# Performance work log

Hardware: AMD Instinct MI355X
Metric: run time of the kernel (lower is better)

## Reference

```python
import jax, jax.numpy as jnp
import numpy as np

N_NODES = 100000
N_EDGES = 1600000
N_FEAT = 128
HIDDEN = 128
N_GRAPHS = 64
N_CLASSES = 10
BN_EPS = 1e-5


def setup_inputs() -> dict:
    key = jax.random.key(0)
    ks = jax.random.split(key, 24)
    glorot = lambda k, o, i: jax.random.normal(k, (o, i), jnp.float32) * (1.0 / np.sqrt(i))
    inp = {
        'x': jax.random.normal(ks[0], (N_NODES, N_FEAT), jnp.float32),
        'edge_index': jax.random.randint(ks[1], (2, N_EDGES), 0, N_NODES, jnp.int64),
        'batch': jnp.sort(jax.random.randint(ks[2], (N_NODES,), 0, N_GRAPHS, jnp.int64)),
        # GCNConv(128 -> 128)
        'gcn_w': glorot(ks[3], HIDDEN, N_FEAT),
        'gcn_b': jnp.zeros((HIDDEN,), jnp.float32),
        # SAGEConv layers 1, 2: lin_l (aggregated, with bias) + lin_r (root, no bias)
        'sage1_wl': glorot(ks[4], HIDDEN, HIDDEN),
        'sage1_bl': jnp.zeros((HIDDEN,), jnp.float32),
        'sage1_wr': glorot(ks[5], HIDDEN, HIDDEN),
        'sage2_wl': glorot(ks[6], HIDDEN, HIDDEN),
        'sage2_bl': jnp.zeros((HIDDEN,), jnp.float32),
        'sage2_wr': glorot(ks[7], HIDDEN, HIDDEN),
        # ClassifierBase: 128 -> 200 -> 100 -> 50 -> 10
        'clf_w0': glorot(ks[8], 200, HIDDEN), 'clf_b0': jnp.zeros((200,), jnp.float32),
        'clf_w1': glorot(ks[9], 100, 200), 'clf_b1': jnp.zeros((100,), jnp.float32),
        'clf_w2': glorot(ks[10], 50, 100), 'clf_b2': jnp.zeros((50,), jnp.float32),
        'clf_w3': glorot(ks[11], N_CLASSES, 50), 'clf_b3': jnp.zeros((N_CLASSES,), jnp.float32),
        # BatchNorm1d (eval mode, running_mean=0, running_var=1)
        'bn0_g': jnp.ones((200,), jnp.float32), 'bn0_b': jnp.zeros((200,), jnp.float32),
        'bn1_g': jnp.ones((100,), jnp.float32), 'bn1_b': jnp.zeros((100,), jnp.float32),
        'bn2_g': jnp.ones((50,), jnp.float32), 'bn2_b': jnp.zeros((50,), jnp.float32),
    }
    return inp


def _gcn_conv(x, src, dst, W, b):
    # PyG GCNConv: add self loops, symmetric deg^{-1/2} normalization
    xw = x @ W.T                                                  # [N, H]
    ones = jnp.ones(src.shape[0], xw.dtype)
    deg = jax.ops.segment_sum(ones, dst, num_segments=N_NODES) + 1.0  # self loops
    dinv = jax.lax.rsqrt(deg)
    norm = dinv[src] * dinv[dst]                                  # [E]
    out = jax.ops.segment_sum(xw[src] * norm[:, None], dst, num_segments=N_NODES)
    out = out + xw * (dinv * dinv)[:, None]                       # self-loop term deg^{-1}
    return out + b


def _sage_conv(x, src, dst, Wl, bl, Wr):
    # PyG SAGEConv (mean aggr): lin_l(mean_{j->i} x_j) + lin_r(x_i)
    ones = jnp.ones(src.shape[0], x.dtype)
    cnt = jax.ops.segment_sum(ones, dst, num_segments=N_NODES)
    agg = jax.ops.segment_sum(x[src], dst, num_segments=N_NODES)
    agg = agg / jnp.maximum(cnt, 1.0)[:, None]
    return agg @ Wl.T + bl + x @ Wr.T


def _bn_eval(h, g, b):
    # eval-mode BatchNorm1d with running_mean=0, running_var=1
    return h * (g / np.sqrt(1.0 + BN_EPS)) + b


def reference(x, edge_index, batch, gcn_w, gcn_b,
              sage1_wl, sage1_bl, sage1_wr, sage2_wl, sage2_bl, sage2_wr,
              clf_w0, clf_b0, clf_w1, clf_b1, clf_w2, clf_b2, clf_w3, clf_b3,
              bn0_g, bn0_b, bn1_g, bn1_b, bn2_g, bn2_b):
    src, dst = edge_index[0], edge_index[1]
    h = _gcn_conv(x, src, dst, gcn_w, gcn_b)          # act_func is None -> no activation
    h = _sage_conv(h, src, dst, sage1_wl, sage1_bl, sage1_wr)
    h = _sage_conv(h, src, dst, sage2_wl, sage2_bl, sage2_wr)
    # global mean pool over graphs
    gcnt = jax.ops.segment_sum(jnp.ones(h.shape[0], h.dtype), batch, num_segments=N_GRAPHS)
    g = jax.ops.segment_sum(h, batch, num_segments=N_GRAPHS) / jnp.maximum(gcnt, 1.0)[:, None]
    # ClassifierBase (eval: dropout inactive), tanh activation
    g = jnp.tanh(_bn_eval(g @ clf_w0.T + clf_b0, bn0_g, bn0_b))
    g = jnp.tanh(_bn_eval(g @ clf_w1.T + clf_b1, bn1_g, bn1_b))
    g = jnp.tanh(_bn_eval(g @ clf_w2.T + clf_b2, bn2_g, bn2_b))
    logits = g @ clf_w3.T + clf_b3
    return jax.nn.softmax(logits, axis=1)             # [B, n_classes]
```

## Files before the change

kernel.cpp:

```cpp
#include <hip/hip_runtime.h>

#define N_NODES 100000
#define N_EDGES 1600000
#define NGRAPH 64
#define NBIN 391
#define EPB 2560
#define NBLK 625
#define WBLK 200
#define CAPB 6144
#define CAPP 7168
#define PSPLIT 8

typedef short s8v __attribute__((ext_vector_type(8)));
typedef float f4v __attribute__((ext_vector_type(4)));
typedef float f2v __attribute__((ext_vector_type(2)));

__device__ __forceinline__ float bflo(unsigned u) { return __uint_as_float(u << 16); }
__device__ __forceinline__ float bfhi(unsigned u) { return __uint_as_float(u & 0xffff0000u); }
__device__ __forceinline__ unsigned short f2bf(float f) {
    unsigned u = __float_as_uint(f);
    u += 0x7fffu + ((u >> 16) & 1u);
    return (unsigned short)(u >> 16);
}
__device__ __forceinline__ float bf2f(unsigned short h) { return __uint_as_float(((unsigned)h) << 16); }
__device__ __forceinline__ unsigned pk(float lo, float hi) {
    return (unsigned)f2bf(lo) | ((unsigned)f2bf(hi) << 16);
}
__device__ __forceinline__ float ldv(const void* p, int i, int f32) {
    return f32 ? ((const float*)p)[i] : bf2f(((const unsigned short*)p)[i]);
}
__device__ __forceinline__ f2v up2(unsigned u) {
    f2v t; t.x = bflo(u); t.y = bfhi(u); return t;
}

__global__ __launch_bounds__(256) void k_prep(const unsigned short* __restrict__ x,
                                              const int* __restrict__ ei,
                                              const int* __restrict__ batch,
                                              int* __restrict__ flags,
                                              int* __restrict__ binCur,
                                              int* __restrict__ gstart,
                                              float* __restrict__ pbuf,
                                              float* __restrict__ wbuf,
                                              unsigned* __restrict__ xcvt,
                                              unsigned* __restrict__ staging,
                                              const void* w0, const void* w1,
                                              const void* w2, const void* w3,
                                              const void* b0, const void* bn0g, const void* bn0b,
                                              const void* b1, const void* bn1g, const void* bn1b,
                                              const void* b2, const void* bn2g, const void* bn2b,
                                              const void* b3) {
    int tid = threadIdx.x, bid = blockIdx.x;
    if (bid < NBLK) {
        __shared__ int cnt[NBIN];
        __shared__ int lofs[NBIN];
        __shared__ int curL[NBIN];
        __shared__ int basg[NBIN];
        __shared__ int sA[512], sB[512];
        __shared__ int sbuf[EPB];
        __shared__ int dbuf[EPB];
        __shared__ unsigned ebuf[EPB];
        __shared__ unsigned short bbuf[EPB];
        __shared__ int p64;
        if (tid == 0) p64 = 0;
        for (int i = tid; i < NBIN; i += 256) cnt[i] = 0;
        __syncthreads();
        if (ei[2 * (tid * 5000) + 1] == 0) atomicAdd(&p64, 1);
        __syncthreads();
        int i64 = (p64 == 256);
        int base = bid * EPB;
        #pragma unroll
        for (int k = 0; k < EPB / 512; ++k) {
            int e = base + k * 512 + tid * 2;
            int s0, s1, d0, d1;
            if (i64) {
                uint4 vs = *(const uint4*)(ei + 2 * (size_t)e);
                uint4 vd = *(const uint4*)(ei + 2 * (size_t)(N_EDGES + e));
                s0 = (int)vs.x; s1 = (int)vs.z;
                d0 = (int)vd.x; d1 = (int)vd.z;
            } else {
                int2 vs = *(const int2*)(ei + (size_t)e);
                int2 vd = *(const int2*)(ei + (size_t)N_EDGES + e);
                s0 = vs.x; s1 = vs.y;
                d0 = vd.x; d1 = vd.y;
            }
            int l = k * 512 + tid * 2;
            sbuf[l] = s0; sbuf[l + 1] = s1;
            dbuf[l] = d0; dbuf[l + 1] = d1;
            if ((unsigned)d0 < N_NODES) atomicAdd(&cnt[d0 >> 8], 1);
            if ((unsigned)d1 < N_NODES) atomicAdd(&cnt[d1 >> 8], 1);
        }
        __syncthreads();
        for (int k = tid; k < 512; k += 256) sA[k] = (k < NBIN) ? cnt[k] : 0;
        __syncthreads();
        int* src = sA;
        int* dst = sB;
        for (int off = 1; off < 512; off <<= 1) {
            for (int k = tid; k < 512; k += 256)
                dst[k] = src[k] + ((k >= off) ? src[k - off] : 0);
            __syncthreads();
            int* t = src; src = dst; dst = t;
        }
        int totE = src[NBIN - 1];
        for (int i = tid; i < NBIN; i += 256) {
            int excl = src[i] - cnt[i];
            lofs[i] = excl;
            curL[i] = excl;
            basg[i] = i * CAPB + (cnt[i] ? atomicAdd(&binCur[i], cnt[i]) : 0);
        }
        __syncthreads();
        #pragma unroll
        for (int k = 0; k < EPB / 256; ++k) {
            int l = k * 256 + tid;
            int d = dbuf[l];
            int s = sbuf[l];
            if ((unsigned)d < N_NODES) {
                s = min(max(s, 0), N_NODES - 1);
                int p = atomicAdd(&curL[d >> 8], 1);
                ebuf[p] = ((unsigned)(d & 255) << 20) | (unsigned)s;
                bbuf[p] = (unsigned short)(d >> 8);
            }
        }
        __syncthreads();
        for (int i = tid; i < totE; i += 256) {
            int bb = bbuf[i];
            int p = basg[bb] + (i - lofs[bb]);
            if (p < (bb + 1) * CAPB) staging[p] = ebuf[i];
        }
        return;
    }
    int wb = bid - NBLK;
    __shared__ int c0, c2;
    if (tid == 0) { c0 = 0; c2 = 0; }
    __syncthreads();
    unsigned short hh = x[tid * 37];
    int e = (hh >> 7) & 0xFF;
    if (e >= 100 && e <= 150) atomicAdd(&c0, 1);
    if (wb == 0 && batch[2 * (tid * 193) + 1] == 0) atomicAdd(&c2, 1);
    __syncthreads();
    int f = (c0 == 256) ? 0 : 1;
    int i = wb * 256 + tid;
    if (i < 25600) wbuf[i] = ldv(w0, i, f);
    else if (i < 45600) wbuf[i] = ldv(w1, i - 25600, f);
    else if (i < 50600) wbuf[i] = ldv(w2, i - 45600, f);
    else if (i < 51100) wbuf[i] = ldv(w3, i - 50600, f);
    if (f) {
        for (int id = wb * 256 + tid; id < N_NODES * 64; id += WBLK * 256) {
            float2 u = ((const float2*)x)[id];
            xcvt[id] = pk(u.x, u.y);
        }
    }
    if (wb != 0) return;
    int b64 = (c2 == 256) ? 1 : 0;
    if (tid == 0) {
        flags[0] = f;
        flags[1] = 0;
        flags[2] = b64;
    }
    if (tid <= NGRAPH) {
        int g = tid, lo = 0, hi = N_NODES;
        while (lo < hi) {
            int mid = (lo + hi) >> 1;
            int v = b64 ? batch[2 * mid] : batch[mid];
            if (v < g) lo = mid + 1;
            else hi = mid;
        }
        gstart[g] = lo;
    }
    const float invs = rsqrtf(1.0f + 1e-5f);
    if (tid < 200) {
        float a = ldv(bn0g, tid, f) * invs;
        pbuf[tid] = a;
        pbuf[200 + tid] = ldv(b0, tid, f) * a + ldv(bn0b, tid, f);
    }
    if (tid < 100) {
        float a = ldv(bn1g, tid, f) * invs;
        pbuf[400 + tid] = a;
        pbuf[500 + tid] = ldv(b1, tid, f) * a + ldv(bn1b, tid, f);
    }
    if (tid < 50) {
        float a = ldv(bn2g, tid, f) * invs;
        pbuf[600 + tid] = a;
        pbuf[650 + tid] = ldv(b2, tid, f) * a + ldv(bn2b, tid, f);
    }
    if (tid < 10) pbuf[700 + tid] = ldv(b3, tid, f);
}

__global__ __launch_bounds__(256) void k_csr(const unsigned* __restrict__ staging,
                                             const int* __restrict__ binCur,
                                             int2* __restrict__ rse,
                                             float* __restrict__ dinv,
                                             int* __restrict__ colidx,
                                             unsigned* __restrict__ padA,
                                             unsigned* __restrict__ padB) {
    __shared__ int deg[256];
    __shared__ int s[256];
    __shared__ int cur[256];
    __shared__ int colbuf[CAPP];
    int b = blockIdx.x, tid = threadIdx.x;
    int n0 = b << 8;
    int nend = min(256, N_NODES - n0);
    int runStart = b * CAPB;
    int outStart = b * CAPP;
    int runLen = min(binCur[b], CAPB);
    deg[tid] = 0;
    for (int i = tid; i < CAPP; i += 256) colbuf[i] = N_NODES;
    __syncthreads();
    for (int i = tid; i < runLen; i += 256)
        atomicAdd(&deg[staging[runStart + i] >> 20], 1);
    __syncthreads();
    int myDeg = deg[tid];
    int pdeg = (myDeg + 15) & ~15;
    s[tid] = pdeg;
    __syncthreads();
    for (int off = 1; off < 256; off <<= 1) {
        int x2 = (tid >= off) ? s[tid - off] : 0;
        __syncthreads();
        s[tid] += x2;
        __syncthreads();
    }
    int incl = s[tid];
    int lrs = incl - pdeg;
    if (tid < nend) {
        rse[n0 + tid] = make_int2(outStart + lrs, outStart + lrs + myDeg);
        dinv[n0 + tid] = rsqrtf((float)myDeg + 1.0f);
    }
    cur[tid] = lrs;
    __syncthreads();
    for (int i = tid; i < runLen; i += 256) {
        unsigned e = staging[runStart + i];
        int p = atomicAdd(&cur[e >> 20], 1);
        if (p < CAPP) colbuf[p] = (int)(e & 0xFFFFF);
    }
    __syncthreads();
    int ptot = min(s[255], CAPP);
    for (int i = tid; i < ptot; i += 256) colidx[outStart + i] = colbuf[i];
    if (b == 0) {
        if (tid < 64) {
            padA[(size_t)N_NODES * 64 + tid] = 0u;
            padB[(size_t)N_NODES * 64 + tid] = 0u;
        }
        if (tid == 0) dinv[N_NODES] = 0.f;
    }
}

template <int MODE>
__global__ __launch_bounds__(256) void k_agg(const uint4* __restrict__ xsA,
                                             const uint4* __restrict__ xsB,
                                             const int2* __restrict__ rse,
                                             const float* __restrict__ dinv,
                                             unsigned* __restrict__ out,
                                             const int* __restrict__ col,
                                             const int* __restrict__ flags) {
    int lane = threadIdx.x & 63;
    int wid = blockIdx.x * 4 + (threadIdx.x >> 6);
    int glane = lane & 15, grp = lane >> 4;
    const uint4* xs = (MODE == 0) ? (flags[0] ? xsB : xsA) : xsA;
    #pragma unroll
    for (int h = 0; h < 2; ++h) {
        int nodeA = wid * 4 + h * 2;
        int nodeB = nodeA + 1;
        int2 ra = rse[nodeA];
        int2 rb = rse[nodeB];
        int degA = ra.y - ra.x, degB = rb.y - rb.x;
        int pendA = ra.x + ((degA + 15) & ~15);
        int pendB = rb.x + ((degB + 15) & ~15);
        int rounds = max(pendA - ra.x, pendB - rb.x) >> 4;
        int baseA = ra.x + grp * 4, baseB = rb.x + grp * 4;
        f2v aA0 = {0.f, 0.f}, aA1 = {0.f, 0.f}, aA2 = {0.f, 0.f}, aA3 = {0.f, 0.f};
        f2v aB0 = {0.f, 0.f}, aB1 = {0.f, 0.f}, aB2 = {0.f, 0.f}, aB3 = {0.f, 0.f};
        uint4 selfA = make_uint4(0u, 0u, 0u, 0u), selfB = make_uint4(0u, 0u, 0u, 0u);
        float diA = 0.f, diB = 0.f;
        if (MODE == 0) {
            selfA = xs[(size_t)nodeA * 16u + glane]; diA = dinv[nodeA];
            selfB = xs[(size_t)nodeB * 16u + glane]; diB = dinv[nodeB];
        }
        for (int r = 0; r < rounds; ++r) {
            int4 ca = *(const int4*)(col + baseA);
            int4 cb = *(const int4*)(col + baseB);
            if (baseA >= pendA) { ca.x = N_NODES; ca.y = N_NODES; ca.z = N_NODES; ca.w = N_NODES; }
            if (baseB >= pendB) { cb.x = N_NODES; cb.y = N_NODES; cb.z = N_NODES; cb.w = N_NODES; }
            baseA += 16; baseB += 16;
            float d0, d1, d2, d3, e0, e1, e2, e3;
            if (MODE == 0) {
                d0 = dinv[ca.x]; d1 = dinv[ca.y]; d2 = dinv[ca.z]; d3 = dinv[ca.w];
                e0 = dinv[cb.x]; e1 = dinv[cb.y]; e2 = dinv[cb.z]; e3 = dinv[cb.w];
                ca.x = min(ca.x, N_NODES - 1); ca.y = min(ca.y, N_NODES - 1);
                ca.z = min(ca.z, N_NODES - 1); ca.w = min(ca.w, N_NODES - 1);
                cb.x = min(cb.x, N_NODES - 1); cb.y = min(cb.y, N_NODES - 1);
                cb.z = min(cb.z, N_NODES - 1); cb.w = min(cb.w, N_NODES - 1);
            }
            uint4 u0 = xs[(size_t)(unsigned)ca.x * 16u + glane];
            uint4 u1 = xs[(size_t)(unsigned)ca.y * 16u + glane];
            uint4 u2 = xs[(size_t)(unsigned)ca.z * 16u + glane];
            uint4 u3 = xs[(size_t)(unsigned)ca.w * 16u + glane];
            uint4 v0 = xs[(size_t)(unsigned)cb.x * 16u + glane];
            uint4 v1 = xs[(size_t)(unsigned)cb.y * 16u + glane];
            uint4 v2 = xs[(size_t)(unsigned)cb.z * 16u + glane];
            uint4 v3 = xs[(size_t)(unsigned)cb.w * 16u + glane];
            if (MODE == 0) {
                aA0 += d0 * up2(u0.x); aA1 += d0 * up2(u0.y); aA2 += d0 * up2(u0.z); aA3 += d0 * up2(u0.w);
                aA0 += d1 * up2(u1.x); aA1 += d1 * up2(u1.y); aA2 += d1 * up2(u1.z); aA3 += d1 * up2(u1.w);
                aA0 += d2 * up2(u2.x); aA1 += d2 * up2(u2.y); aA2 += d2 * up2(u2.z); aA3 += d2 * up2(u2.w);
                aA0 += d3 * up2(u3.x); aA1 += d3 * up2(u3.y); aA2 += d3 * up2(u3.z); aA3 += d3 * up2(u3.w);
                aB0 += e0 * up2(v0.x); aB1 += e0 * up2(v0.y); aB2 += e0 * up2(v0.z); aB3 += e0 * up2(v0.w);
                aB0 += e1 * up2(v1.x); aB1 += e1 * up2(v1.y); aB2 += e1 * up2(v1.z); aB3 += e1 * up2(v1.w);
                aB0 += e2 * up2(v2.x); aB1 += e2 * up2(v2.y); aB2 += e2 * up2(v2.z); aB3 += e2 * up2(v2.w);
                aB0 += e3 * up2(v3.x); aB1 += e3 * up2(v3.y); aB2 += e3 * up2(v3.z); aB3 += e3 * up2(v3.w);
            } else {
                aA0 += up2(u0.x); aA1 += up2(u0.y); aA2 += up2(u0.z); aA3 += up2(u0.w);
                aA0 += up2(u1.x); aA1 += up2(u1.y); aA2 += up2(u1.z); aA3 += up2(u1.w);
                aA0 += up2(u2.x); aA1 += up2(u2.y); aA2 += up2(u2.z); aA3 += up2(u2.w);
                aA0 += up2(u3.x); aA1 += up2(u3.y); aA2 += up2(u3.z); aA3 += up2(u3.w);
                aB0 += up2(v0.x); aB1 += up2(v0.y); aB2 += up2(v0.z); aB3 += up2(v0.w);
                aB0 += up2(v1.x); aB1 += up2(v1.y); aB2 += up2(v1.z); aB3 += up2(v1.w);
                aB0 += up2(v2.x); aB1 += up2(v2.y); aB2 += up2(v2.z); aB3 += up2(v2.w);
                aB0 += up2(v3.x); aB1 += up2(v3.y); aB2 += up2(v3.z); aB3 += up2(v3.w);
            }
        }
        float rA[8] = {aA0.x, aA0.y, aA1.x, aA1.y, aA2.x, aA2.y, aA3.x, aA3.y};
        float rB[8] = {aB0.x, aB0.y, aB1.x, aB1.y, aB2.x, aB2.y, aB3.x, aB3.y};
        #pragma unroll
        for (int i = 0; i < 8; ++i) {
            float v = rA[i];
            v += __shfl_xor(v, 16, 64);
            v += __shfl_xor(v, 32, 64);
            rA[i] = v;
            float w = rB[i];
            w += __shfl_xor(w, 16, 64);
            w += __shfl_xor(w, 32, 64);
            rB[i] = w;
        }
        if (MODE == 0) {
            float dA2 = diA * diA, dB2 = diB * diB;
            rA[0] = diA * rA[0] + dA2 * bflo(selfA.x); rA[1] = diA * rA[1] + dA2 * bfhi(selfA.x);
            rA[2] = diA * rA[2] + dA2 * bflo(selfA.y); rA[3] = diA * rA[3] + dA2 * bfhi(selfA.y);
            rA[4] = diA * rA[4] + dA2 * bflo(selfA.z); rA[5] = diA * rA[5] + dA2 * bfhi(selfA.z);
            rA[6] = diA * rA[6] + dA2 * bflo(selfA.w); rA[7] = diA * rA[7] + dA2 * bfhi(selfA.w);
            rB[0] = diB * rB[0] + dB2 * bflo(selfB.x); rB[1] = diB * rB[1] + dB2 * bfhi(selfB.x);
            rB[2] = diB * rB[2] + dB2 * bflo(selfB.y); rB[3] = diB * rB[3] + dB2 * bfhi(selfB.y);
            rB[4] = diB * rB[4] + dB2 * bflo(selfB.z); rB[5] = diB * rB[5] + dB2 * bfhi(selfB.z);
            rB[6] = diB * rB[6] + dB2 * bflo(selfB.w); rB[7] = diB * rB[7] + dB2 * bfhi(selfB.w);
        } else {
            float sA = 1.0f / fmaxf((float)degA, 1.0f);
            float sB = 1.0f / fmaxf((float)degB, 1.0f);
            #pragma unroll
            for (int i = 0; i < 8; ++i) { rA[i] *= sA; rB[i] *= sB; }
        }
        if (grp == 0) {
            uint4 o;
            o.x = pk(rA[0], rA[1]); o.y = pk(rA[2], rA[3]);
            o.z = pk(rA[4], rA[5]); o.w = pk(rA[6], rA[7]);
            *(uint4*)(out + (size_t)nodeA * 64 + glane * 4) = o;
            o.x = pk(rB[0], rB[1]); o.y = pk(rB[2], rB[3]);
            o.z = pk(rB[4], rB[5]); o.w = pk(rB[6], rB[7]);
            *(uint4*)(out + (size_t)nodeB * 64 + glane * 4) = o;
        }
    }
}

template <int DUAL>
__global__ __launch_bounds__(512) void k_gemm(const unsigned short* __restrict__ A0,
                                              const void* __restrict__ W0,
                                              const unsigned short* __restrict__ A1,
                                              const void* __restrict__ W1,
                                              const void* __restrict__ bias,
                                              unsigned short* __restrict__ out,
                                              const int* __restrict__ flags) {
    __shared__ __align__(16) unsigned short Ws[128][136];
    int f32 = flags[0];
    int tid = threadIdx.x;
    int lane = tid & 63;
    int wave = tid >> 6;
    int rowbase = blockIdx.x * 128;
    int lr = lane & 15, q = lane >> 4;
    int m0 = wave * 16;
    int arow = rowbase + m0 + lr;
    if (arow > N_NODES) arow = N_NODES;

    f4v acc[8];
    #pragma unroll
    for (int t = 0; t < 8; ++t) acc[t] = (f4v){0.f, 0.f, 0.f, 0.f};

    #pragma unroll
    for (int p = 0; p < (DUAL ? 2 : 1); ++p) {
        const unsigned short* Ap = p ? A1 : A0;
        const void* Wp = p ? W1 : W0;
        if (p) __syncthreads();
        if (!f32) {
            const unsigned short* Wf = (const unsigned short*)Wp;
            #pragma unroll
            for (int it = 0; it < 4; ++it) {
                int chunk = tid + it * 512;
                int r = chunk >> 4, c8 = (chunk & 15) * 8;
                *(uint4*)&Ws[r][c8] = *(const uint4*)(Wf + r * 128 + c8);
            }
        } else {
            const float* Wf = (const float*)Wp;
            #pragma unroll
            for (int it = 0; it < 8; ++it) {
                int chunk = tid + it * 512;
                int r = chunk >> 5, c4 = (chunk & 31) * 4;
                float4 v = *(const float4*)(Wf + r * 128 + c4);
                *(uint2*)&Ws[r][c4] = make_uint2(pk(v.x, v.y), pk(v.z, v.w));
            }
        }
        const unsigned short* Arp = Ap + (size_t)arow * 128;
        s8v a[4];
        #pragma unroll
        for (int k = 0; k < 4; ++k) a[k] = *(const s8v*)(Arp + k * 32 + q * 8);
        __syncthreads();
        #pragma unroll
        for (int k = 0; k < 4; ++k) {
            #pragma unroll
            for (int t = 0; t < 8; ++t) {
                s8v b = *(const s8v*)&Ws[t * 16 + lr][k * 32 + q * 8];
                acc[t] = __builtin_amdgcn_mfma_f32_16x16x32_bf16(a[k], b, acc[t], 0, 0, 0);
            }
        }
    }
    #pragma unroll
    for (int t = 0; t < 8; ++t) {
        int o = t * 16 + lr;
        float bv = ldv(bias, o, f32);
        #pragma unroll
        for (int j = 0; j < 4; ++j) {
            int m = rowbase + m0 + q * 4 + j;
            if (m < N_NODES) out[(size_t)m * 128 + o] = f2bf(acc[t][j] + bv);
        }
    }
}

__global__ __launch_bounds__(256) void k_pool2(const unsigned* __restrict__ h,
                                               const int* __restrict__ gstart,
                                               float* __restrict__ ppool) {
    __shared__ float part[4][128];
    int g = blockIdx.x / PSPLIT, sl = blockIdx.x % PSPLIT;
    int wave = threadIdx.x >> 6, lane = threadIdx.x & 63;
    int s0 = gstart[g], s1 = gstart[g + 1];
    int n = s1 - s0;
    int chunk = (n + PSPLIT - 1) / PSPLIT;
    int r0 = s0 + sl * chunk;
    int r1 = min(r0 + chunk, s1);
    float a0 = 0.f, a1 = 0.f;
    for (int r = r0 + wave; r < r1; r += 4) {
        unsigned u = h[(size_t)r * 64 + lane];
        a0 += bflo(u);
        a1 += bfhi(u);
    }
    part[wave][2 * lane] = a0;
    part[wave][2 * lane + 1] = a1;
    __syncthreads();
    int t = threadIdx.x;
    if (t < 128) {
        float s = part[0][t] + part[1][t] + part[2][t] + part[3][t];
        ppool[(size_t)blockIdx.x * 128 + t] = s;
    }
}

__global__ __launch_bounds__(256) void k_clf(const float* __restrict__ ppool,
                                             const int* __restrict__ gstart,
                                             const float* __restrict__ wbuf,
                                             const float* __restrict__ pbuf,
                                             void* outv, const int* __restrict__ flags) {
    __shared__ float gin[128];
    __shared__ float ha[200];
    __shared__ float hb[100];
    int b = blockIdx.x, t = threadIdx.x;
    if (t < 128) {
        float s = 0.f;
        #pragma unroll
        for (int k = 0; k < PSPLIT; ++k) s += ppool[(size_t)(b * PSPLIT + k) * 128 + t];
        int cnt = gstart[b + 1] - gstart[b];
        gin[t] = s / fmaxf((float)cnt, 1.0f);
    }
    __syncthreads();
    if (t < 200) {
        const float4* wr = (const float4*)(wbuf + t * 128);
        float s = 0.f;
        #pragma unroll
        for (int k = 0; k < 32; ++k) {
            float4 v = wr[k];
            s += v.x * gin[4 * k] + v.y * gin[4 * k + 1] + v.z * gin[4 * k + 2] + v.w * gin[4 * k + 3];
        }
        ha[t] = tanhf(s * pbuf[t] + pbuf[200 + t]);
    }
    __syncthreads();
    if (t < 100) {
        const float4* wr = (const float4*)(wbuf + 25600 + t * 200);
        float s = 0.f;
        #pragma unroll
        for (int k = 0; k < 50; ++k) {
            float4 v = wr[k];
            s += v.x * ha[4 * k] + v.y * ha[4 * k + 1] + v.z * ha[4 * k + 2] + v.w * ha[4 * k + 3];
        }
        hb[t] = tanhf(s * pbuf[400 + t] + pbuf[500 + t]);
    }
    __syncthreads();
    if (t < 50) {
        const float4* wr = (const float4*)(wbuf + 45600 + t * 100);
        float s = 0.f;
        #pragma unroll
        for (int k = 0; k < 25; ++k) {
            float4 v = wr[k];
            s += v.x * hb[4 * k] + v.y * hb[4 * k + 1] + v.z * hb[4 * k + 2] + v.w * hb[4 * k + 3];
        }
        gin[t] = tanhf(s * pbuf[600 + t] + pbuf[650 + t]);
    }
    __syncthreads();
    if (t == 0) {
        int f = flags[0];
        float lg[10];
        float mx = -1e30f;
        #pragma unroll
        for (int c = 0; c < 10; ++c) {
            const float* wr = wbuf + 50600 + c * 50;
            float s = 0.f;
            for (int k = 0; k < 50; ++k) s += wr[k] * gin[k];
            s += pbuf[700 + c];
            lg[c] = s;
            mx = fmaxf(mx, s);
        }
        float sum = 0.f;
        #pragma unroll
        for (int c = 0; c < 10; ++c) {
            lg[c] = __expf(lg[c] - mx);
            sum += lg[c];
        }
        float inv = 1.0f / sum;
        #pragma unroll
        for (int c = 0; c < 10; ++c) {
            float v = lg[c] * inv;
            if (f) ((float*)outv)[b * 10 + c] = v;
            else ((unsigned short*)outv)[b * 10 + c] = f2bf(v);
        }
    }
}

extern "C" void kernel_launch(void* const* d_in, const int* in_sizes, int n_in,
                              void* d_out, int out_size, void* d_ws, size_t ws_size,
                              hipStream_t stream) {
    const unsigned short* x16 = (const unsigned short*)d_in[0];
    const int* ei = (const int*)d_in[1];
    const int* batch = (const int*)d_in[2];

    char* ws = (char*)d_ws;
    size_t off = 0;
    auto alloc = [&](size_t bytes) {
        size_t r = off;
        off = (off + bytes + 255) & ~(size_t)255;
        return r;
    };
    int* flags = (int*)(ws + alloc(256));
    int2* rse = (int2*)(ws + alloc((size_t)N_NODES * 8));
    int* colidx = (int*)(ws + alloc((size_t)NBIN * CAPP * 4 + (size_t)CAPP * 4));
    float* dinv = (float*)(ws + alloc((size_t)(N_NODES + 1) * 4));
    int* binCur = (int*)(ws + alloc(NBIN * 4));
    int* gstart = (int*)(ws + alloc((NGRAPH + 1) * 4));
    float* pbuf = (float*)(ws + alloc(710 * 4));
    float* ppool = (float*)(ws + alloc((size_t)NGRAPH * PSPLIT * 128 * 4));
    float* wbuf = (float*)(ws + alloc(51100 * 4));
    unsigned short* bufA = (unsigned short*)(ws + alloc((size_t)(N_NODES + 1) * 128 * 2));
    unsigned short* bufB = (unsigned short*)(ws + alloc((size_t)(N_NODES + 1) * 128 * 2));
    unsigned* staging = (unsigned*)bufA;

    hipMemsetAsync(binCur, 0, NBIN * 4, stream);
    k_prep<<<NBLK + WBLK, 256, 0, stream>>>(x16, ei, batch, flags, binCur, gstart, pbuf, wbuf,
                                            (unsigned*)bufB, staging,
                                            d_in[11], d_in[13], d_in[15], d_in[17],
                                            d_in[12], d_in[19], d_in[20],
                                            d_in[14], d_in[21], d_in[22],
                                            d_in[16], d_in[23], d_in[24], d_in[18]);
    k_csr<<<NBIN, 256, 0, stream>>>(staging, binCur, rse, dinv, colidx,
                                    (unsigned*)bufA, (unsigned*)bufB);

    k_agg<0><<<N_NODES / 16, 256, 0, stream>>>((const uint4*)x16, (const uint4*)bufB,
                                               rse, dinv, (unsigned*)bufA, colidx, flags);
    k_gemm<0><<<(N_NODES + 127) / 128, 512, 0, stream>>>(bufA, d_in[3], nullptr, nullptr,
                                                         d_in[4], bufA, flags);
    k_agg<1><<<N_NODES / 16, 256, 0, stream>>>((const uint4*)bufA, (const uint4*)bufA,
                                               rse, dinv, (unsigned*)bufB, colidx, flags);
    k_gemm<1><<<(N_NODES + 127) / 128, 512, 0, stream>>>(bufB, d_in[5], bufA, d_in[7],
                                                         d_in[6], bufB, flags);
    k_agg<1><<<N_NODES / 16, 256, 0, stream>>>((const uint4*)bufB, (const uint4*)bufB,
                                               rse, dinv, (unsigned*)bufA, colidx, flags);
    k_gemm<1><<<(N_NODES + 127) / 128, 512, 0, stream>>>(bufA, d_in[8], bufB, d_in[10],
                                                         d_in[9], bufA, flags);
    k_pool2<<<NGRAPH * PSPLIT, 256, 0, stream>>>((const unsigned*)bufA, gstart, ppool);
    k_clf<<<NGRAPH, 256, 0, stream>>>(ppool, gstart, wbuf, pbuf, d_out, flags);
}
```

Measured before the change: 488.6 us.

## Split prep kernel into setup and lean edge-binning kernels, drop memset

The fused prep kernel is split into a setup kernel (dtype detection, weight/param prep, x conversion, binCur zeroing) and a separate binfill kernel that bins edges by destination. Binfill uses less shared memory: it drops the local sort and staging buffers, scatters directly to global staging via shared atomics, and re-reads source indices instead of caching them. This should raise occupancy and removes a memset launch, but adds a kernel launch, a serial dependency, and less coalesced global writes.

```diff
diff --git a/kernel.cpp b/kernel.cpp
--- a/kernel.cpp
+++ b/kernel.cpp
@@ -6,10 +6,10 @@
 #define NBIN 391
 #define EPB 2560
 #define NBLK 625
-#define WBLK 200
 #define CAPB 6144
 #define CAPP 7168
 #define PSPLIT 8
+#define SETUPBLK 1600
 
 typedef short s8v __attribute__((ext_vector_type(8)));
 typedef float f4v __attribute__((ext_vector_type(4)));
@@ -33,129 +33,53 @@
     f2v t; t.x = bflo(u); t.y = bfhi(u); return t;
 }
 
-__global__ __launch_bounds__(256) void k_prep(const unsigned short* __restrict__ x,
-                                              const int* __restrict__ ei,
-                                              const int* __restrict__ batch,
-                                              int* __restrict__ flags,
-                                              int* __restrict__ binCur,
-                                              int* __restrict__ gstart,
-                                              float* __restrict__ pbuf,
-                                              float* __restrict__ wbuf,
-                                              unsigned* __restrict__ xcvt,
-                                              unsigned* __restrict__ staging,
-                                              const void* w0, const void* w1,
-                                              const void* w2, const void* w3,
-                                              const void* b0, const void* bn0g, const void* bn0b,
-                                              const void* b1, const void* bn1g, const void* bn1b,
-                                              const void* b2, const void* bn2g, const void* bn2b,
-                                              const void* b3) {
+__global__ __launch_bounds__(256) void k_setup(const unsigned short* __restrict__ x,
+                                               const int* __restrict__ ei,
+                                               const int* __restrict__ batch,
+                                               int* __restrict__ flags,
+                                               int* __restrict__ binCur,
+                                               int* __restrict__ gstart,
+                                               float* __restrict__ pbuf,
+                                               float* __restrict__ wbuf,
+                                               unsigned* __restrict__ xcvt,
+                                               const void* w0, const void* w1,
+                                               const void* w2, const void* w3,
+                                               const void* b0, const void* bn0g, const void* bn0b,
+                                               const void* b1, const void* bn1g, const void* bn1b,
+                                               const void* b2, const void* bn2g, const void* bn2b,
+                                               const void* b3) {
+    __shared__ int cnt[3];
     int tid = threadIdx.x, bid = blockIdx.x;
-    if (bid < NBLK) {
-        __shared__ int cnt[NBIN];
-        __shared__ int lofs[NBIN];
-        __shared__ int curL[NBIN];
-        __shared__ int basg[NBIN];
-        __shared__ int sA[512], sB[512];
-        __shared__ int sbuf[EPB];
-        __shared__ int dbuf[EPB];
-        __shared__ unsigned ebuf[EPB];
-        __shared__ unsigned short bbuf[EPB];
-        __shared__ int p64;
-        if (tid == 0) p64 = 0;
-        for (int i = tid; i < NBIN; i += 256) cnt[i] = 0;
-        __syncthreads();
-        if (ei[2 * (tid * 5000) + 1] == 0) atomicAdd(&p64, 1);
-        __syncthreads();
-        int i64 = (p64 == 256);
-        int base = bid * EPB;
-        #pragma unroll
-        for (int k = 0; k < EPB / 512; ++k) {
-            int e = base + k * 512 + tid * 2;
-            int s0, s1, d0, d1;
-            if (i64) {
-                uint4 vs = *(const uint4*)(ei + 2 * (size_t)e);
-                uint4 vd = *(const uint4*)(ei + 2 * (size_t)(N_EDGES + e));
-                s0 = (int)vs.x; s1 = (int)vs.z;
-                d0 = (int)vd.x; d1 = (int)vd.z;
-            } else {
-                int2 vs = *(const int2*)(ei + (size_t)e);
-                int2 vd = *(const int2*)(ei + (size_t)N_EDGES + e);
-                s0 = vs.x; s1 = vs.y;
-                d0 = vd.x; d1 = vd.y;
-            }
-            int l = k * 512 + tid * 2;
-            sbuf[l] = s0; sbuf[l + 1] = s1;
-            dbuf[l] = d0; dbuf[l + 1] = d1;
-            if ((unsigned)d0 < N_NODES) atomicAdd(&cnt[d0 >> 8], 1);
-            if ((unsigned)d1 < N_NODES) atomicAdd(&cnt[d1 >> 8], 1);
-        }
-        __syncthreads();
-        for (int k = tid; k < 512; k += 256) sA[k] = (k < NBIN) ? cnt[k] : 0;
-        __syncthreads();
-        int* src = sA;
-        int* dst = sB;
-        for (int off = 1; off < 512; off <<= 1) {
-            for (int k = tid; k < 512; k += 256)
-                dst[k] = src[k] + ((k >= off) ? src[k - off] : 0);
-            __syncthreads();
-            int* t = src; src = dst; dst = t;
-        }
-        int totE = src[NBIN - 1];
-        for (int i = tid; i < NBIN; i += 256) {
-            int excl = src[i] - cnt[i];
-            lofs[i] = excl;
-            curL[i] = excl;
-            basg[i] = i * CAPB + (cnt[i] ? atomicAdd(&binCur[i], cnt[i]) : 0);
-        }
-        __syncthreads();
-        #pragma unroll
-        for (int k = 0; k < EPB / 256; ++k) {
-            int l = k * 256 + tid;
-            int d = dbuf[l];
-            int s = sbuf[l];
-            if ((unsigned)d < N_NODES) {
-                s = min(max(s, 0), N_NODES - 1);
-                int p = atomicAdd(&curL[d >> 8], 1);
-                ebuf[p] = ((unsigned)(d & 255) << 20) | (unsigned)s;
-                bbuf[p] = (unsigned short)(d >> 8);
-            }
-        }
-        __syncthreads();
-        for (int i = tid; i < totE; i += 256) {
-            int bb = bbuf[i];
-            int p = basg[bb] + (i - lofs[bb]);
-            if (p < (bb + 1) * CAPB) staging[p] = ebuf[i];
-        }
-        return;
-    }
-    int wb = bid - NBLK;
-    __shared__ int c0, c2;
-    if (tid == 0) { c0 = 0; c2 = 0; }
-    __syncthreads();
-    unsigned short hh = x[tid * 37];
-    int e = (hh >> 7) & 0xFF;
-    if (e >= 100 && e <= 150) atomicAdd(&c0, 1);
-    if (wb == 0 && batch[2 * (tid * 193) + 1] == 0) atomicAdd(&c2, 1);
-    __syncthreads();
-    int f = (c0 == 256) ? 0 : 1;
-    int i = wb * 256 + tid;
+    if (tid < 3) cnt[tid] = 0;
+    __syncthreads();
+    unsigned short h = x[tid * 37];
+    int e = (h >> 7) & 0xFF;
+    if (e >= 100 && e <= 150) atomicAdd(&cnt[0], 1);
+    if (bid == 0) {
+        if (ei[2 * (tid * 5000) + 1] == 0) atomicAdd(&cnt[1], 1);
+        if (batch[2 * (tid * 193) + 1] == 0) atomicAdd(&cnt[2], 1);
+    }
+    __syncthreads();
+    int f = (cnt[0] == 256) ? 0 : 1;
+    int i = bid * 256 + tid;
     if (i < 25600) wbuf[i] = ldv(w0, i, f);
     else if (i < 45600) wbuf[i] = ldv(w1, i - 25600, f);
     else if (i < 50600) wbuf[i] = ldv(w2, i - 45600, f);
     else if (i < 51100) wbuf[i] = ldv(w3, i - 50600, f);
     if (f) {
-        for (int id = wb * 256 + tid; id < N_NODES * 64; id += WBLK * 256) {
+        for (int id = bid * 256 + tid; id < N_NODES * 64; id += SETUPBLK * 256) {
             float2 u = ((const float2*)x)[id];
             xcvt[id] = pk(u.x, u.y);
         }
     }
-    if (wb != 0) return;
-    int b64 = (c2 == 256) ? 1 : 0;
+    if (bid != 0) return;
+    int b64 = (cnt[2] == 256) ? 1 : 0;
     if (tid == 0) {
         flags[0] = f;
-        flags[1] = 0;
+        flags[1] = (cnt[1] == 256) ? 1 : 0;
         flags[2] = b64;
     }
+    for (int k = tid; k < NBIN; k += 256) binCur[k] = 0;
     if (tid <= NGRAPH) {
         int g = tid, lo = 0, hi = N_NODES;
         while (lo < hi) {
@@ -183,6 +107,69 @@
         pbuf[650 + tid] = ldv(b2, tid, f) * a + ldv(bn2b, tid, f);
     }
     if (tid < 10) pbuf[700 + tid] = ldv(b3, tid, f);
+}
+
+__global__ __launch_bounds__(256) void k_binfill(const int* __restrict__ ei,
+                                                 int* __restrict__ binCur,
+                                                 unsigned* __restrict__ staging,
+                                                 const int* __restrict__ flags) {
+    __shared__ int cnt[NBIN];
+    __shared__ int basg[NBIN];
+    __shared__ int dbuf[EPB];
+    int tid = threadIdx.x;
+    int i64 = flags[1];
+    int base = blockIdx.x * EPB;
+    for (int i = tid; i < NBIN; i += 256) cnt[i] = 0;
+    __syncthreads();
+    #pragma unroll
+    for (int k = 0; k < EPB / 512; ++k) {
+        int e = base + k * 512 + tid * 2;
+        int d0, d1;
+        if (i64) {
+            uint4 vd = *(const uint4*)(ei + 2 * (size_t)(N_EDGES + e));
+            d0 = (int)vd.x; d1 = (int)vd.z;
+        } else {
+            int2 vd = *(const int2*)(ei + (size_t)N_EDGES + e);
+            d0 = vd.x; d1 = vd.y;
+        }
+        int l = k * 512 + tid * 2;
+        dbuf[l] = d0; dbuf[l + 1] = d1;
+        if ((unsigned)d0 < N_NODES) atomicAdd(&cnt[d0 >> 8], 1);
+        if ((unsigned)d1 < N_NODES) atomicAdd(&cnt[d1 >> 8], 1);
+    }
+    __syncthreads();
+    for (int i = tid; i < NBIN; i += 256) {
+        int c = cnt[i];
+        basg[i] = i * CAPB + (c ? atomicAdd(&binCur[i], c) : 0);
+        cnt[i] = 0;
+    }
+    __syncthreads();
+    #pragma unroll
+    for (int k = 0; k < EPB / 512; ++k) {
+        int e = base + k * 512 + tid * 2;
+        int s0, s1;
+        if (i64) {
+            uint4 vs = *(const uint4*)(ei + 2 * (size_t)e);
+            s0 = (int)vs.x; s1 = (int)vs.z;
+        } else {
+            int2 vs = *(const int2*)(ei + (size_t)e);
+            s0 = vs.x; s1 = vs.y;
+        }
+        int l = k * 512 + tid * 2;
+        #pragma unroll
+        for (int hh = 0; hh < 2; ++hh) {
+            int d = dbuf[l + hh];
+            int s = hh ? s1 : s0;
+            if ((unsigned)d < N_NODES) {
+                s = min(max(s, 0), N_NODES - 1);
+                int b = d >> 8;
+                int p = atomicAdd(&cnt[b], 1);
+                int pos = basg[b] + p;
+                if (pos < (b + 1) * CAPB)
+                    staging[pos] = ((unsigned)(d & 255) << 20) | (unsigned)s;
+            }
+        }
+    }
 }
 
 __global__ __launch_bounds__(256) void k_csr(const unsigned* __restrict__ staging,
@@ -563,13 +550,14 @@
     unsigned short* bufB = (unsigned short*)(ws + alloc((size_t)(N_NODES + 1) * 128 * 2));
     unsigned* staging = (unsigned*)bufA;
 
-    hipMemsetAsync(binCur, 0, NBIN * 4, stream);
-    k_prep<<<NBLK + WBLK, 256, 0, stream>>>(x16, ei, batch, flags, binCur, gstart, pbuf, wbuf,
-                                            (unsigned*)bufB, staging,
-                                            d_in[11], d_in[13], d_in[15], d_in[17],
-                                            d_in[12], d_in[19], d_in[20],
-                                            d_in[14], d_in[21], d_in[22],
-                                            d_in[16], d_in[23], d_in[24], d_in[18]);
+    k_setup<<<SETUPBLK, 256, 0, stream>>>(x16, ei, batch, flags, binCur, gstart, pbuf, wbuf,
+                                          (unsigned*)bufB,
+                                          d_in[11], d_in[13], d_in[15], d_in[17],
+                                          d_in[12], d_in[19], d_in[20],
+                                          d_in[14], d_in[21], d_in[22],
+                                          d_in[16], d_in[23], d_in[24], d_in[18]);
+
+    k_binfill<<<NBLK, 256, 0, stream>>>(ei, binCur, staging, flags);
     k_csr<<<NBIN, 256, 0, stream>>>(staging, binCur, rse, dinv, colidx,
                                     (unsigned*)bufA, (unsigned*)bufB);
 
```

Measured after the change: 472.0 us. -3.4%, faster.
